# Kernel tuning notes

Hardware: AMD Instinct MI355X
Metric: run time of the kernel (lower is better)

## Reference

```python
import jax, jax.numpy as jnp
import numpy as np

N = 4096
F_IN = 512
F_OUT = 64
HEADS = 8
ALPHA = 0.2  # LeakyReLU negative slope
NEG_INF = -9e15


def setup_inputs() -> dict:
    key = jax.random.key(0)
    k1, k2, k3, k4 = jax.random.split(key, 4)
    x = jax.random.normal(k1, (N, F_IN), dtype=jnp.float32)
    adj = jax.random.randint(k2, (N, N), 0, 2, dtype=jnp.int32)  # dense 0/1 adjacency
    # xavier_uniform with gain=1.414 per head
    limW = 1.414 * float(np.sqrt(6.0 / (F_IN + F_OUT)))
    lima = 1.414 * float(np.sqrt(6.0 / (2 * F_OUT + 1)))
    W = jax.random.uniform(k3, (HEADS, F_IN, F_OUT), minval=-limW, maxval=limW, dtype=jnp.float32)
    a = jax.random.uniform(k4, (HEADS, 2 * F_OUT), minval=-lima, maxval=lima, dtype=jnp.float32)
    return {"x": x, "adj": adj, "W": W, "a": a}


def reference(x, adj, W, a):
    # Per-head linear: Wh [H, N, F_OUT]
    Wh = jnp.einsum("nf,hfo->hno", x, W)
    # Pairwise concat + matmul with a decomposes into f1_i + f2_j
    f1 = jnp.einsum("hno,ho->hn", Wh, a[:, :F_OUT])  # [H, N]
    f2 = jnp.einsum("hno,ho->hn", Wh, a[:, F_OUT:])  # [H, N]
    e = jax.nn.leaky_relu(f1[:, :, None] + f2[:, None, :], ALPHA)  # [H, N, N]
    e = jnp.where(adj[None, :, :] > 0, e, NEG_INF)
    attn = jax.nn.softmax(e, axis=-1)  # masked row softmax; dropout is eval-mode identity
    out = jnp.einsum("hnm,hmo->hno", attn, Wh)  # weighted aggregation
    # concat heads: [N, H*F_OUT]
    return jnp.transpose(out, (1, 0, 2)).reshape(N, HEADS * F_OUT)
```

## Files before the change

kernel.cpp:

```cpp
#include <hip/hip_runtime.h>
#include <hip/hip_bf16.h>

#define NN   4096
#define FIN  512
#define FOUT 64
#define NH   8
#define ALPHA 0.2f
#define ROWS 128
#define LOG2E 1.4426950408889634f

typedef __attribute__((ext_vector_type(8))) short bf16x8;
typedef __attribute__((ext_vector_type(4))) float f32x4;

__device__ __forceinline__ unsigned short f2bf(float x) {
    unsigned u = __float_as_uint(x);
    return (unsigned short)((u + 0x7fffu + ((u >> 16) & 1u)) >> 16);
}

__device__ __forceinline__ unsigned pk2(float a, float b) {
    union { __hip_bfloat162 h2; unsigned u; } cv;
    cv.h2 = __float22bfloat162_rn(float2{a, b});
    return cv.u;
}

__global__ __launch_bounds__(256) void kb(const int* __restrict__ adj,
                                          unsigned long long* __restrict__ bits) {
    const int wv   = blockIdx.x * 4 + (threadIdx.x >> 6);
    const int lane = threadIdx.x & 63;
    const int base = wv * 32;
    #pragma unroll
    for (int r = 0; r < 4; ++r) {
        int v0 = adj[(size_t)(base + r*8 + 0) * 64 + lane];
        int v1 = adj[(size_t)(base + r*8 + 1) * 64 + lane];
        int v2 = adj[(size_t)(base + r*8 + 2) * 64 + lane];
        int v3 = adj[(size_t)(base + r*8 + 3) * 64 + lane];
        int v4 = adj[(size_t)(base + r*8 + 4) * 64 + lane];
        int v5 = adj[(size_t)(base + r*8 + 5) * 64 + lane];
        int v6 = adj[(size_t)(base + r*8 + 6) * 64 + lane];
        int v7 = adj[(size_t)(base + r*8 + 7) * 64 + lane];
        unsigned long long m0 = __ballot(v0 > 0);
        unsigned long long m1 = __ballot(v1 > 0);
        unsigned long long m2 = __ballot(v2 > 0);
        unsigned long long m3 = __ballot(v3 > 0);
        unsigned long long m4 = __ballot(v4 > 0);
        unsigned long long m5 = __ballot(v5 > 0);
        unsigned long long m6 = __ballot(v6 > 0);
        unsigned long long m7 = __ballot(v7 > 0);
        if (lane == 0) {
            ulonglong2* dst = (ulonglong2*)&bits[base + r*8];
            dst[0] = {m0, m1};
            dst[1] = {m2, m3};
            dst[2] = {m4, m5};
            dst[3] = {m6, m7};
        }
    }
}

__global__ __launch_bounds__(256) void kg(const float* __restrict__ x,
                                          const float* __restrict__ W,
                                          const float* __restrict__ aw,
                                          unsigned short* __restrict__ WhTs,
                                          float* __restrict__ f1,
                                          float* __restrict__ f2) {
    __shared__ float As[16][68];
    __shared__ float Bs[16][68];
    __shared__ unsigned short Tb[64][80];
    __shared__ float r1[64][16];
    __shared__ float r2[64][16];
    const int t = threadIdx.x;
    const int bx   = blockIdx.x;
    const int h    = bx >> 6;
    const int nti  = bx & 63;
    const int row0 = nti * 64;
    const int tr = t >> 4, tc = t & 15;
    const int ar = t >> 2, ak = t & 3;
    const int bk = t >> 4, bo = t & 15;
    const float* WH = W + (size_t)h * FIN * FOUT;
    float acc[4][4] = {};

    for (int k0i = 0; k0i < FIN; k0i += 16) {
        __syncthreads();
        float4 av = *(const float4*)&x[(size_t)(row0 + ar) * FIN + k0i + ak * 4];
        As[ak*4+0][ar] = av.x; As[ak*4+1][ar] = av.y;
        As[ak*4+2][ar] = av.z; As[ak*4+3][ar] = av.w;
        *(float4*)&Bs[bk][bo*4] =
            *(const float4*)&WH[(size_t)(k0i + bk) * FOUT + bo*4];
        __syncthreads();
        #pragma unroll
        for (int kk = 0; kk < 16; ++kk) {
            float4 a4 = *(const float4*)&As[kk][tr*4];
            float4 b4 = *(const float4*)&Bs[kk][tc*4];
            float a[4] = {a4.x, a4.y, a4.z, a4.w};
            float b[4] = {b4.x, b4.y, b4.z, b4.w};
            #pragma unroll
            for (int i = 0; i < 4; ++i)
                #pragma unroll
                for (int j = 0; j < 4; ++j)
                    acc[i][j] = fmaf(a[i], b[j], acc[i][j]);
        }
    }

    float a1v[4], a2v[4];
    #pragma unroll
    for (int j = 0; j < 4; ++j) {
        a1v[j] = aw[h * 2 * FOUT + tc*4 + j];
        a2v[j] = aw[h * 2 * FOUT + FOUT + tc*4 + j];
    }
    #pragma unroll
    for (int i = 0; i < 4; ++i) {
        float s1 = 0.f, s2 = 0.f;
        #pragma unroll
        for (int j = 0; j < 4; ++j) {
            s1 = fmaf(acc[i][j], a1v[j], s1);
            s2 = fmaf(acc[i][j], a2v[j], s2);
            Tb[tc*4 + j][tr*4 + i] = f2bf(acc[i][j]);
        }
        r1[tr*4 + i][tc] = s1;
        r2[tr*4 + i][tc] = s2;
    }
    __syncthreads();
    if (t < 64) {
        float s1 = 0.f, s2 = 0.f;
        #pragma unroll
        for (int k = 0; k < 16; ++k) { s1 += r1[t][k]; s2 += r2[t][k]; }
        f1[h * NN + row0 + t] = s1 * LOG2E;
        f2[h * NN + row0 + t] = s2 * LOG2E;
    }
    unsigned char* tileB = (unsigned char*)(WhTs + ((size_t)(h * 64) + nti) * 4096);
    #pragma unroll
    for (int i = 0; i < 2; ++i) {
        int c = t + i * 256;
        int o = c >> 3, nch = c & 7;
        *(uint4*)(tileB + o * 128 + ((nch * 16) ^ ((o & 7) << 4))) =
            *(const uint4*)&Tb[o][nch * 8];
    }
}

__global__ __launch_bounds__(512, 8) void k3_attn(
        const unsigned long long* __restrict__ bits,
        const unsigned short* __restrict__ WhTs,
        const float* __restrict__ f1, const float* __restrict__ f2,
        float* __restrict__ pnum, float* __restrict__ pden) {
    __shared__ unsigned char psB[ROWS * 128];
    __shared__ unsigned char wsB[8192];
    const int t    = threadIdx.x;
    const int lane = t & 63, wid = t >> 6;
    const int h    = blockIdx.y;
    const int row0 = blockIdx.x * ROWS;
    const int js   = blockIdx.z, JS = gridDim.z;
    const int ntile = (NN / 64) / JS;
    const int nt0   = js * ntile;
    const int pr   = t >> 2, psub = t & 3;
    const float f1r = f1[h * NN + row0 + pr];
    const float* f2h = f2 + h * NN;
    const unsigned long long* bitsRow = bits + (size_t)(row0 + pr) * 64;
    const unsigned short* WTS = WhTs + (size_t)h * 64 * 4096;
    const int prswz = (pr & 7) << 4;
    f32x4 acc[4] = {};
    f32x4 accd = {};
    const bf16x8 ones = {0x3F80, 0x3F80, 0x3F80, 0x3F80,
                         0x3F80, 0x3F80, 0x3F80, 0x3F80};

    uint4 wreg;
    auto loadW = [&](int nti, uint4& w0) {
        w0 = ((const uint4*)(WTS + (size_t)nti * 4096))[t];
    };
    loadW(nt0, wreg);

    const int kb2 = (lane >> 4) * 16;
    for (int it = 0; it < ntile; ++it) {
        const int nti = nt0 + it;
        __syncthreads();
        *(uint4*)&wsB[t * 16] = wreg;
        {
            unsigned msk = (unsigned)(bitsRow[nti] >> (psub << 4)) & 0xFFFFu;
            const float* f2c = f2h + nti * 64 + psub * 16;
            #pragma unroll
            for (int half = 0; half < 2; ++half) {
                unsigned pk[4];
                #pragma unroll
                for (int c2 = 0; c2 < 2; ++c2) {
                    const int c = half * 2 + c2;
                    float4 f4 = *(const float4*)&f2c[c * 4];
                    float e0 = f1r + f4.x, e1 = f1r + f4.y;
                    float e2 = f1r + f4.z, e3 = f1r + f4.w;
                    e0 = fmaxf(e0, ALPHA * e0); e1 = fmaxf(e1, ALPHA * e1);
                    e2 = fmaxf(e2, ALPHA * e2); e3 = fmaxf(e3, ALPHA * e3);
                    const int b = c * 4;
                    float p0 = ((msk >> (b+0)) & 1u) ? __builtin_amdgcn_exp2f(e0) : 0.f;
                    float p1 = ((msk >> (b+1)) & 1u) ? __builtin_amdgcn_exp2f(e1) : 0.f;
                    float p2 = ((msk >> (b+2)) & 1u) ? __builtin_amdgcn_exp2f(e2) : 0.f;
                    float p3 = ((msk >> (b+3)) & 1u) ? __builtin_amdgcn_exp2f(e3) : 0.f;
                    pk[c2*2+0] = pk2(p0, p1);
                    pk[c2*2+1] = pk2(p2, p3);
                }
                uint4 w = {pk[0], pk[1], pk[2], pk[3]};
                *(uint4*)&psB[pr * 128 + ((psub*32 + half*16) ^ prswz)] = w;
            }
        }
        if (it + 1 < ntile) loadW(nti + 1, wreg);
        __syncthreads();
        {
            const int arw  = wid * 16 + (lane & 15);
            const int aswz = (arw & 7) << 4;
            #pragma unroll
            for (int ks = 0; ks < 2; ++ks) {
                bf16x8 af = *(const bf16x8*)&psB[arw * 128 + ((ks*64 + kb2) ^ aswz)];
                accd = __builtin_amdgcn_mfma_f32_16x16x32_bf16(af, ones, accd, 0, 0, 0);
                #pragma unroll
                for (int cf = 0; cf < 4; ++cf) {
                    int brw = cf * 16 + (lane & 15);
                    bf16x8 bfr = *(const bf16x8*)&wsB[brw * 128 + ((ks*64 + kb2) ^ ((brw & 7) << 4))];
                    acc[cf] = __builtin_amdgcn_mfma_f32_16x16x32_bf16(af, bfr, acc[cf], 0, 0, 0);
                }
            }
        }
    }

    float* pn = pnum + (((size_t)js * NH + h) * NN + row0) * 64;
    #pragma unroll
    for (int cf = 0; cf < 4; ++cf) {
        int o = cf * 16 + (lane & 15);
        #pragma unroll
        for (int rg = 0; rg < 4; ++rg) {
            int rl = wid * 16 + (lane >> 4) * 4 + rg;
            pn[(size_t)rl * 64 + o] = acc[cf][rg];
        }
    }
    if ((lane & 15) == 0) {
        float* pd = pden + ((size_t)js * NH + h) * NN + row0;
        #pragma unroll
        for (int rg = 0; rg < 4; ++rg)
            pd[wid * 16 + (lane >> 4) * 4 + rg] = accd[rg];
    }
}

__global__ __launch_bounds__(256) void k4_red(const float* __restrict__ pnum,
                                              const float* __restrict__ pden,
                                              float* __restrict__ out, int JS) {
    const int idx = blockIdx.x * 256 + threadIdx.x;
    const int h   = idx >> 16;
    const int rem = idx & 65535;
    const int n   = rem >> 4;
    const int o4  = (rem & 15) * 4;
    float4 s = {0.f, 0.f, 0.f, 0.f};
    float  d = 0.f;
    for (int js = 0; js < JS; ++js) {
        const float* p = pnum + (((size_t)js * NH + h) * NN + n) * 64 + o4;
        float4 v = *(const float4*)p;
        s.x += v.x; s.y += v.y; s.z += v.z; s.w += v.w;
        d += pden[((size_t)js * NH + h) * NN + n];
    }
    float inv = 1.0f / d;
    float4 r = {s.x * inv, s.y * inv, s.z * inv, s.w * inv};
    *(float4*)&out[(size_t)n * (NH * FOUT) + h * FOUT + o4] = r;
}

extern "C" void kernel_launch(void* const* d_in, const int* in_sizes, int n_in,
                              void* d_out, int out_size, void* d_ws, size_t ws_size,
                              hipStream_t stream) {
    const float* x   = (const float*)d_in[0];
    const int*   adj = (const int*)d_in[1];
    const float* W   = (const float*)d_in[2];
    const float* a   = (const float*)d_in[3];
    float* outp = (float*)d_out;

    unsigned short* WhTs = (unsigned short*)d_ws;
    float* f1 = (float*)(WhTs + (size_t)NH * 64 * NN);
    float* f2 = f1 + NH * NN;
    unsigned long long* bits = (unsigned long long*)(f2 + NH * NN);
    float* pnum = (float*)(bits + (size_t)NN * 64);
    const size_t baseBytes  = (size_t)(pnum - (float*)d_ws) * 4;
    const size_t sliceBytes = (size_t)NH * NN * 65 * 4;
    int JS = 1;
    if (ws_size >= baseBytes + 4 * sliceBytes) JS = 4;
    else if (ws_size >= baseBytes + 2 * sliceBytes) JS = 2;
    float* pden = pnum + (size_t)JS * NH * NN * 64;

    kb     <<<dim3(2048),            256, 0, stream>>>(adj, bits);
    kg     <<<dim3(512),             256, 0, stream>>>(x, W, a, WhTs, f1, f2);
    k3_attn<<<dim3(NN/ROWS, NH, JS), 512, 0, stream>>>(bits, WhTs, f1, f2, pnum, pden);
    k4_red <<<dim3(NN*NH*FOUT/4/256), 256, 0, stream>>>(pnum, pden, outp, JS);
}
```

Before: 112.3 us.

## Factor exp of leaky-relu into per-node exponentials and build MFMA A operand in registers

Uses exp(leaky(f1+f2)) = max(e^f1*e^f2, e^{a f1}*e^{a f2}) to precompute per-node exponentials in kg, replacing per-pair exp2 in the attention kernel with two multiplies and a max. Each lane now computes directly the probabilities its MFMA A fragment needs, so the psB shared-memory staging buffer and its reads are removed. This reduces transcendental work and LDS traffic, but doubles global reads of the per-column factors. It also risks overflow or precision loss because there is no max-subtraction and exponentials of large logits are multiplied directly.

```diff
diff --git a/kernel.cpp b/kernel.cpp
--- a/kernel.cpp
+++ b/kernel.cpp
@@ -60,8 +60,10 @@
                                           const float* __restrict__ W,
                                           const float* __restrict__ aw,
                                           unsigned short* __restrict__ WhTs,
-                                          float* __restrict__ f1,
-                                          float* __restrict__ f2) {
+                                          float* __restrict__ E1,
+                                          float* __restrict__ F1,
+                                          float* __restrict__ E2,
+                                          float* __restrict__ F2) {
     __shared__ float As[16][68];
     __shared__ float Bs[16][68];
     __shared__ unsigned short Tb[64][80];
@@ -123,8 +125,11 @@
         float s1 = 0.f, s2 = 0.f;
         #pragma unroll
         for (int k = 0; k < 16; ++k) { s1 += r1[t][k]; s2 += r2[t][k]; }
-        f1[h * NN + row0 + t] = s1 * LOG2E;
-        f2[h * NN + row0 + t] = s2 * LOG2E;
+        float a = s1 * LOG2E, b = s2 * LOG2E;
+        E1[h * NN + row0 + t] = __builtin_amdgcn_exp2f(a);
+        F1[h * NN + row0 + t] = __builtin_amdgcn_exp2f(ALPHA * a);
+        E2[h * NN + row0 + t] = __builtin_amdgcn_exp2f(b);
+        F2[h * NN + row0 + t] = __builtin_amdgcn_exp2f(ALPHA * b);
     }
     unsigned char* tileB = (unsigned char*)(WhTs + ((size_t)(h * 64) + nti) * 4096);
     #pragma unroll
@@ -139,9 +144,9 @@
 __global__ __launch_bounds__(512, 8) void k3_attn(
         const unsigned long long* __restrict__ bits,
         const unsigned short* __restrict__ WhTs,
-        const float* __restrict__ f1, const float* __restrict__ f2,
+        const float* __restrict__ E1, const float* __restrict__ F1,
+        const float* __restrict__ E2, const float* __restrict__ F2,
         float* __restrict__ pnum, float* __restrict__ pden) {
-    __shared__ unsigned char psB[ROWS * 128];
     __shared__ unsigned char wsB[8192];
     const int t    = threadIdx.x;
     const int lane = t & 63, wid = t >> 6;
@@ -150,12 +155,14 @@
     const int js   = blockIdx.z, JS = gridDim.z;
     const int ntile = (NN / 64) / JS;
     const int nt0   = js * ntile;
-    const int pr   = t >> 2, psub = t & 3;
-    const float f1r = f1[h * NN + row0 + pr];
-    const float* f2h = f2 + h * NN;
-    const unsigned long long* bitsRow = bits + (size_t)(row0 + pr) * 64;
+    const int myrow = wid * 16 + (lane & 15);
+    const int kq    = lane >> 4;
+    const float E1r = E1[h * NN + row0 + myrow];
+    const float F1r = F1[h * NN + row0 + myrow];
+    const float* E2h = E2 + h * NN;
+    const float* F2h = F2 + h * NN;
+    const unsigned long long* bitsRow = bits + (size_t)(row0 + myrow) * 64;
     const unsigned short* WTS = WhTs + (size_t)h * 64 * 4096;
-    const int prswz = (pr & 7) << 4;
     f32x4 acc[4] = {};
     f32x4 accd = {};
     const bf16x8 ones = {0x3F80, 0x3F80, 0x3F80, 0x3F80,
@@ -167,51 +174,42 @@
     };
     loadW(nt0, wreg);
 
-    const int kb2 = (lane >> 4) * 16;
     for (int it = 0; it < ntile; ++it) {
         const int nti = nt0 + it;
         __syncthreads();
         *(uint4*)&wsB[t * 16] = wreg;
+        const unsigned long long m64 = bitsRow[nti];
+        union { uint4 u; bf16x8 v; } af[2];
+        #pragma unroll
+        for (int ks = 0; ks < 2; ++ks) {
+            const int c0 = nti * 64 + ks * 32 + kq * 8;
+            float4 ea = *(const float4*)&E2h[c0];
+            float4 eb = *(const float4*)&E2h[c0 + 4];
+            float4 fa = *(const float4*)&F2h[c0];
+            float4 fb = *(const float4*)&F2h[c0 + 4];
+            const unsigned mb = (unsigned)(m64 >> (ks * 32 + kq * 8)) & 0xFFu;
+            float p0 = (mb &   1u) ? fmaxf(E1r * ea.x, F1r * fa.x) : 0.f;
+            float p1 = (mb &   2u) ? fmaxf(E1r * ea.y, F1r * fa.y) : 0.f;
+            float p2 = (mb &   4u) ? fmaxf(E1r * ea.z, F1r * fa.z) : 0.f;
+            float p3 = (mb &   8u) ? fmaxf(E1r * ea.w, F1r * fa.w) : 0.f;
+            float p4 = (mb &  16u) ? fmaxf(E1r * eb.x, F1r * fb.x) : 0.f;
+            float p5 = (mb &  32u) ? fmaxf(E1r * eb.y, F1r * fb.y) : 0.f;
+            float p6 = (mb &  64u) ? fmaxf(E1r * eb.z, F1r * fb.z) : 0.f;
+            float p7 = (mb & 128u) ? fmaxf(E1r * eb.w, F1r * fb.w) : 0.f;
+            af[ks].u = uint4{pk2(p0, p1), pk2(p2, p3), pk2(p4, p5), pk2(p6, p7)};
+        }
+        if (it + 1 < ntile) loadW(nti + 1, wreg);
+        __syncthreads();
         {
-            unsigned msk = (unsigned)(bitsRow[nti] >> (psub << 4)) & 0xFFFFu;
-            const float* f2c = f2h + nti * 64 + psub * 16;
-            #pragma unroll
-            for (int half = 0; half < 2; ++half) {
-                unsigned pk[4];
-                #pragma unroll
-                for (int c2 = 0; c2 < 2; ++c2) {
-                    const int c = half * 2 + c2;
-                    float4 f4 = *(const float4*)&f2c[c * 4];
-                    float e0 = f1r + f4.x, e1 = f1r + f4.y;
-                    float e2 = f1r + f4.z, e3 = f1r + f4.w;
-                    e0 = fmaxf(e0, ALPHA * e0); e1 = fmaxf(e1, ALPHA * e1);
-                    e2 = fmaxf(e2, ALPHA * e2); e3 = fmaxf(e3, ALPHA * e3);
-                    const int b = c * 4;
-                    float p0 = ((msk >> (b+0)) & 1u) ? __builtin_amdgcn_exp2f(e0) : 0.f;
-                    float p1 = ((msk >> (b+1)) & 1u) ? __builtin_amdgcn_exp2f(e1) : 0.f;
-                    float p2 = ((msk >> (b+2)) & 1u) ? __builtin_amdgcn_exp2f(e2) : 0.f;
-                    float p3 = ((msk >> (b+3)) & 1u) ? __builtin_amdgcn_exp2f(e3) : 0.f;
-                    pk[c2*2+0] = pk2(p0, p1);
-                    pk[c2*2+1] = pk2(p2, p3);
-                }
-                uint4 w = {pk[0], pk[1], pk[2], pk[3]};
-                *(uint4*)&psB[pr * 128 + ((psub*32 + half*16) ^ prswz)] = w;
-            }
-        }
-        if (it + 1 < ntile) loadW(nti + 1, wreg);
-        __syncthreads();
-        {
-            const int arw  = wid * 16 + (lane & 15);
-            const int aswz = (arw & 7) << 4;
+            const int kbyte = kq * 16;
             #pragma unroll
             for (int ks = 0; ks < 2; ++ks) {
-                bf16x8 af = *(const bf16x8*)&psB[arw * 128 + ((ks*64 + kb2) ^ aswz)];
-                accd = __builtin_amdgcn_mfma_f32_16x16x32_bf16(af, ones, accd, 0, 0, 0);
+                accd = __builtin_amdgcn_mfma_f32_16x16x32_bf16(af[ks].v, ones, accd, 0, 0, 0);
                 #pragma unroll
                 for (int cf = 0; cf < 4; ++cf) {
                     int brw = cf * 16 + (lane & 15);
-                    bf16x8 bfr = *(const bf16x8*)&wsB[brw * 128 + ((ks*64 + kb2) ^ ((brw & 7) << 4))];
-                    acc[cf] = __builtin_amdgcn_mfma_f32_16x16x32_bf16(af, bfr, acc[cf], 0, 0, 0);
+                    bf16x8 bfr = *(const bf16x8*)&wsB[brw * 128 + ((ks*64 + kbyte) ^ ((brw & 7) << 4))];
+                    acc[cf] = __builtin_amdgcn_mfma_f32_16x16x32_bf16(af[ks].v, bfr, acc[cf], 0, 0, 0);
                 }
             }
         }
@@ -266,11 +264,13 @@
     float* outp = (float*)d_out;
 
     unsigned short* WhTs = (unsigned short*)d_ws;
-    float* f1 = (float*)(WhTs + (size_t)NH * 64 * NN);
-    float* f2 = f1 + NH * NN;
-    unsigned long long* bits = (unsigned long long*)(f2 + NH * NN);
+    float* E1 = (float*)(WhTs + (size_t)NH * 64 * NN);
+    float* F1 = E1 + NH * NN;
+    float* E2 = F1 + NH * NN;
+    float* F2 = E2 + NH * NN;
+    unsigned long long* bits = (unsigned long long*)(F2 + NH * NN);
     float* pnum = (float*)(bits + (size_t)NN * 64);
-    const size_t baseBytes  = (size_t)(pnum - (float*)d_ws) * 4;
+    const size_t baseBytes  = (size_t)((char*)pnum - (char*)d_ws);
     const size_t sliceBytes = (size_t)NH * NN * 65 * 4;
     int JS = 1;
     if (ws_size >= baseBytes + 4 * sliceBytes) JS = 4;
@@ -278,7 +278,7 @@
     float* pden = pnum + (size_t)JS * NH * NN * 64;
 
     kb     <<<dim3(2048),            256, 0, stream>>>(adj, bits);
-    kg     <<<dim3(512),             256, 0, stream>>>(x, W, a, WhTs, f1, f2);
-    k3_attn<<<dim3(NN/ROWS, NH, JS), 512, 0, stream>>>(bits, WhTs, f1, f2, pnum, pden);
+    kg     <<<dim3(512),             256, 0, stream>>>(x, W, a, WhTs, E1, F1, E2, F2);
+    k3_attn<<<dim3(NN/ROWS, NH, JS), 512, 0, stream>>>(bits, WhTs, E1, F1, E2, F2, pnum, pden);
     k4_red <<<dim3(NN*NH*FOUT/4/256), 256, 0, stream>>>(pnum, pden, outp, JS);
 }
```

After: 190.3 us. 1.69x slower.
